# Kernel optimization log

Hardware: AMD Instinct MI355X
Metric: run time of the kernel (lower is better)

Reference implementation:

```python
import jax, jax.numpy as jnp
import numpy as np
import math

B = 8192
N_MODELS = 64
T_PER_SPLIT = 16
MAXLEAF = 64
EMB = 32
BN_EPS = 1e-5


def setup_inputs() -> dict:
    key = jax.random.key(0)
    k1, k2, k3 = jax.random.split(key, 3)
    # leaf indices per (sample, model*tree), values in [0, maxleaf)
    x = jax.random.randint(k1, (B, N_MODELS * T_PER_SPLIT), 0, MAXLEAF, dtype=jnp.int32)
    # embed_w ~ N(0, sqrt(1/max_ntree_per_split))
    embed_w = jax.random.normal(k2, (N_MODELS, T_PER_SPLIT * MAXLEAF, EMB), dtype=jnp.float32) * math.sqrt(1.0 / T_PER_SPLIT)
    # BatchNorm1d affine params (gamma=1, beta=0 at init)
    bn_gamma = jnp.ones((N_MODELS * EMB,), dtype=jnp.float32)
    bn_beta = jnp.zeros((N_MODELS * EMB,), dtype=jnp.float32)
    # BatchDense(n_models, embsize, 1): weight (M, E, 1) squeezed to (M, E), bias zeros (M,)
    stdv = math.sqrt(6.0 / (EMB + 1))
    bout_w = jax.random.uniform(k3, (N_MODELS, EMB), dtype=jnp.float32, minval=-stdv, maxval=stdv)
    bout_b = jnp.zeros((N_MODELS,), dtype=jnp.float32)
    return {"x": x, "embed_w": embed_w, "bn_gamma": bn_gamma, "bn_beta": bn_beta,
            "bout_w": bout_w, "bout_b": bout_b}


def reference(x, embed_w, bn_gamma, bn_beta, bout_w, bout_b):
    # x: (B, M*T) int leaf indices; embed_w: (M, T*L, E)
    Bn = x.shape[0]
    M, TL, E = embed_w.shape
    T = x.shape[1] // M
    L = TL // T
    # one_hot + bmm == per-tree gather from embed_w, summed over trees
    idx = x.reshape(Bn, M, T) + jnp.arange(T, dtype=x.dtype) * L  # (B, M, T) into TL axis
    emb = embed_w[jnp.arange(M)[None, :, None], idx]              # (B, M, T, E) gather
    h = emb.sum(axis=2).reshape(Bn, M * E)                        # (B, M*E)
    # BatchNorm1d (training-mode batch statistics, biased variance as in torch)
    mean = h.mean(axis=0)
    var = h.var(axis=0)
    h = (h - mean) / jnp.sqrt(var + BN_EPS) * bn_gamma + bn_beta
    # dropout is identity in eval mode
    h = h.reshape(Bn, M, E)
    # BatchDense: per-model linear E -> 1
    out = jnp.einsum('bme,me->bm', h, bout_w) + bout_b            # (B, M)
    sum_out = out.sum(axis=-1, keepdims=True)                     # (B, 1)
    return (sum_out, out)
```

## Files before the change

kernel.cpp:

```cpp
#include <hip/hip_runtime.h>
#include <hip/hip_fp16.h>

constexpr int B_TOT = 8192;
constexpr int NM    = 64;
constexpr int TT    = 16;
constexpr int LF    = 64;
constexpr int EM    = 32;
constexpr int XROW  = NM * TT;
constexpr int TROWS = TT * LF;

template<int TQ>
__device__ __forceinline__ int4 qbcast(int4 v) {
    constexpr int c = TQ * 0x55;
    int4 r;
    r.x = __builtin_amdgcn_mov_dpp(v.x, c, 0xf, 0xf, true);
    r.y = __builtin_amdgcn_mov_dpp(v.y, c, 0xf, 0xf, true);
    r.z = __builtin_amdgcn_mov_dpp(v.z, c, 0xf, 0xf, true);
    r.w = __builtin_amdgcn_mov_dpp(v.w, c, 0xf, 0xf, true);
    return r;
}

__device__ __forceinline__ __half2 H2(unsigned u) { return *(const __half2*)&u; }

__global__ __launch_bounds__(512, 4) void k_stats_f16(
    const int* __restrict__ x, const float* __restrict__ tbl,
    float* __restrict__ psum, float* __restrict__ psq)
{
    __shared__ uint4 tb[TROWS * 4];
    __shared__ float red[2][8][32];

    const int m     = blockIdx.x & 63;
    const int chunk = blockIdx.x >> 6;
    const int tid   = threadIdx.x;
    const int f     = tid & 3;
    const int grp   = tid >> 2;
    const int b0    = chunk * 1024;

    {
        const float4* __restrict__ src = (const float4*)(tbl + (size_t)m * (TROWS * EM));
#pragma unroll
        for (int i = 0; i < 8; ++i) {
            const int o = tid + i * 512;
            const float4 a = src[o * 2];
            const float4 c = src[o * 2 + 1];
            uint4 p;
            __half2 h0 = __floats2half2_rn(a.x, a.y);
            __half2 h1 = __floats2half2_rn(a.z, a.w);
            __half2 h2 = __floats2half2_rn(c.x, c.y);
            __half2 h3 = __floats2half2_rn(c.z, c.w);
            p.x = *(unsigned*)&h0; p.y = *(unsigned*)&h1;
            p.z = *(unsigned*)&h2; p.w = *(unsigned*)&h3;
            tb[o] = p;
        }
    }

    int4 xr = ((const int4*)(x + (size_t)(b0 + grp) * XROW + m * TT))[f];

    float s[8], s2[8];
#pragma unroll
    for (int k = 0; k < 8; ++k) { s[k] = 0.f; s2[k] = 0.f; }

    __syncthreads();

    for (int p = 0; p < 8; ++p) {
        int4 nxt;
        if (p < 7)
            nxt = ((const int4*)(x + (size_t)(b0 + (p + 1) * 128 + grp) * XROW + m * TT))[f];

        const int4 q0 = qbcast<0>(xr);
        const int4 q1 = qbcast<1>(xr);
        const int4 q2 = qbcast<2>(xr);
        const int4 q3 = qbcast<3>(xr);

        __half2 h0 = __half2(__half(0.f), __half(0.f));
        __half2 h1 = h0, h2 = h0, h3 = h0;

#define GATH(Q, RB)                                                          \
        {                                                                    \
            const uint4 a0 = tb[((Q).x + RB      ) * 4 + f];                 \
            const uint4 a1 = tb[((Q).y + RB +  64) * 4 + f];                 \
            const uint4 a2 = tb[((Q).z + RB + 128) * 4 + f];                 \
            const uint4 a3 = tb[((Q).w + RB + 192) * 4 + f];                 \
            h0 = __hadd2(h0, __hadd2(__hadd2(H2(a0.x), H2(a1.x)),            \
                                     __hadd2(H2(a2.x), H2(a3.x))));          \
            h1 = __hadd2(h1, __hadd2(__hadd2(H2(a0.y), H2(a1.y)),            \
                                     __hadd2(H2(a2.y), H2(a3.y))));          \
            h2 = __hadd2(h2, __hadd2(__hadd2(H2(a0.z), H2(a1.z)),            \
                                     __hadd2(H2(a2.z), H2(a3.z))));          \
            h3 = __hadd2(h3, __hadd2(__hadd2(H2(a0.w), H2(a1.w)),            \
                                     __hadd2(H2(a2.w), H2(a3.w))));          \
        }
        GATH(q0, 0) GATH(q1, 256) GATH(q2, 512) GATH(q3, 768)
#undef GATH

        const __half2 hv[4] = {h0, h1, h2, h3};
#pragma unroll
        for (int k = 0; k < 4; ++k) {
            const float lo = __low2float(hv[k]);
            const float hi = __high2float(hv[k]);
            s[2*k]   += lo;  s2[2*k]   = fmaf(lo, lo, s2[2*k]);
            s[2*k+1] += hi;  s2[2*k+1] = fmaf(hi, hi, s2[2*k+1]);
        }
        xr = nxt;
    }

#pragma unroll
    for (int off = 4; off <= 32; off <<= 1) {
#pragma unroll
        for (int k = 0; k < 8; ++k) {
            s[k]  += __shfl_xor(s[k],  off);
            s2[k] += __shfl_xor(s2[k], off);
        }
    }
    const int wave = tid >> 6;
    if ((tid & 63) < 4) {
#pragma unroll
        for (int k = 0; k < 8; ++k) {
            red[0][wave][f * 8 + k] = s[k];
            red[1][wave][f * 8 + k] = s2[k];
        }
    }
    __syncthreads();
    if (tid < 32) {
        float a = 0.f, a2 = 0.f;
#pragma unroll
        for (int w = 0; w < 8; ++w) { a += red[0][w][tid]; a2 += red[1][w][tid]; }
        psum[(chunk * NM + m) * EM + tid] = a;
        psq [(chunk * NM + m) * EM + tid] = a2;
    }
}

__global__ __launch_bounds__(256) void k_prep(
    const float* __restrict__ tbl,
    const float* __restrict__ gamma, const float* __restrict__ beta,
    const float* __restrict__ bw, const float* __restrict__ bb,
    const float* __restrict__ psum, const float* __restrict__ psq,
    float* __restrict__ Cm, float* __restrict__ g2)
{
    const int m    = blockIdx.x >> 2;
    const int part = blockIdx.x & 3;
    __shared__ float a_s[EM];
    if (threadIdx.x < EM) {
        const int e  = threadIdx.x;
        const int ch = m * EM + e;
        float sum = 0.f, sq = 0.f;
#pragma unroll
        for (int c = 0; c < 8; ++c) {
            sum += psum[(c * NM + m) * EM + e];
            sq  += psq [(c * NM + m) * EM + e];
        }
        const float inv_n = 1.f / (float)B_TOT;
        const float mean = sum * inv_n;
        const float var  = sq * inv_n - mean * mean;
        const float istd = rsqrtf(var + 1e-5f);
        const float g = gamma[ch];
        const float w = bw[ch];
        a_s[e] = istd * g * w;
        float ct = (beta[ch] - mean * istd * g) * w;
#pragma unroll
        for (int off = 16; off > 0; off >>= 1) ct += __shfl_down(ct, off, 32);
        if (e == 0 && part == 0) Cm[m] = bb[m] + ct;
    }
    __syncthreads();

    const float* __restrict__ tblm = tbl + (size_t)m * (TROWS * EM);
    const int row = part * 256 + threadIdx.x;
    const float4* rp = (const float4*)(tblm + row * EM);
    float acc = 0.f;
#pragma unroll
    for (int i = 0; i < 8; ++i) {
        const float4 v = rp[i];
        acc += v.x * a_s[i*4+0] + v.y * a_s[i*4+1]
             + v.z * a_s[i*4+2] + v.w * a_s[i*4+3];
    }
    g2[row * NM + m] = acc;
}

__global__ __launch_bounds__(1024, 8) void k_out(
    const int* __restrict__ x, const float* __restrict__ g2,
    const float* __restrict__ Cm, float* __restrict__ out)
{
    __shared__ float slab[4 * LF * NM];
    const int tid  = threadIdx.x;
    const int wid  = tid >> 6;
    const int lane = tid & 63;
    const int b    = blockIdx.x * 16 + wid;

    const int4* xp = (const int4*)(x + (size_t)b * XROW + lane * TT);
    const int4 q0 = xp[0], q1 = xp[1], q2 = xp[2], q3 = xp[3];
    const int idxs[16] = {q0.x,q0.y,q0.z,q0.w, q1.x,q1.y,q1.z,q1.w,
                          q2.x,q2.y,q2.z,q2.w, q3.x,q3.y,q3.z,q3.w};

    float acc = 0.f;
#pragma unroll
    for (int ph = 0; ph < 4; ++ph) {
        if (ph) __syncthreads();
        const float4* src = (const float4*)(g2 + (size_t)ph * (4 * LF * NM));
        float4* dst = (float4*)slab;
#pragma unroll
        for (int j = 0; j < 4; ++j) dst[tid + j * 1024] = src[tid + j * 1024];
        __syncthreads();
#pragma unroll
        for (int tt = 0; tt < 4; ++tt)
            acc += slab[tt * (LF * NM) + idxs[ph * 4 + tt] * NM + lane];
    }

    const float o = acc + Cm[lane];
    float s = o;
#pragma unroll
    for (int off = 32; off > 0; off >>= 1) s += __shfl_down(s, off);
    out[B_TOT + (size_t)b * NM + lane] = o;
    if (lane == 0) out[b] = s;
}

extern "C" void kernel_launch(void* const* d_in, const int* in_sizes, int n_in,
                              void* d_out, int out_size, void* d_ws, size_t ws_size,
                              hipStream_t stream) {
    const int*   x       = (const int*)d_in[0];
    const float* embed_w = (const float*)d_in[1];
    const float* gamma   = (const float*)d_in[2];
    const float* beta    = (const float*)d_in[3];
    const float* bout_w  = (const float*)d_in[4];
    const float* bout_b  = (const float*)d_in[5];
    float* out = (float*)d_out;

    float* ws   = (float*)d_ws;
    float* Cm   = ws;
    float* g2   = ws + 64;
    float* psum = ws + 64 + 65536;
    float* psq  = psum + 16384;

    k_stats_f16<<<dim3(512), dim3(512), 0, stream>>>(x, embed_w, psum, psq);
    k_prep<<<dim3(256), dim3(256),  0, stream>>>(embed_w, gamma, beta, bout_w,
                                                 bout_b, psum, psq, Cm, g2);
    k_out <<<dim3(512), dim3(1024), 0, stream>>>(x, g2, Cm, out);
}
```

Baseline: 108.6 us.

## Materialize fp16 embeddings in stats pass and apply BN-dense from them

```diff
diff --git a/kernel.cpp b/kernel.cpp
--- a/kernel.cpp
+++ b/kernel.cpp
@@ -24,7 +24,8 @@
 
 __global__ __launch_bounds__(512, 4) void k_stats_f16(
     const int* __restrict__ x, const float* __restrict__ tbl,
-    float* __restrict__ psum, float* __restrict__ psq)
+    float* __restrict__ psum, float* __restrict__ psq,
+    __half* __restrict__ h_out)
 {
     __shared__ uint4 tb[TROWS * 4];
     __shared__ float red[2][8][32];
@@ -50,7 +51,8 @@
             __half2 h3 = __floats2half2_rn(c.z, c.w);
             p.x = *(unsigned*)&h0; p.y = *(unsigned*)&h1;
             p.z = *(unsigned*)&h2; p.w = *(unsigned*)&h3;
-            tb[o] = p;
+            const int sw = (o & ~3) | ((o ^ (o >> 3)) & 3);
+            tb[sw] = p;
         }
     }
 
@@ -59,6 +61,9 @@
     float s[8], s2[8];
 #pragma unroll
     for (int k = 0; k < 8; ++k) { s[k] = 0.f; s2[k] = 0.f; }
+
+    __half* __restrict__ hp =
+        h_out + ((size_t)(b0 + grp) * NM + m) * EM + f * 8;
 
     __syncthreads();
 
@@ -75,12 +80,13 @@
         __half2 h0 = __half2(__half(0.f), __half(0.f));
         __half2 h1 = h0, h2 = h0, h3 = h0;
 
+#define TIX(r) (((r) << 2) | ((f ^ ((r) >> 1)) & 3))
 #define GATH(Q, RB)                                                          \
         {                                                                    \
-            const uint4 a0 = tb[((Q).x + RB      ) * 4 + f];                 \
-            const uint4 a1 = tb[((Q).y + RB +  64) * 4 + f];                 \
-            const uint4 a2 = tb[((Q).z + RB + 128) * 4 + f];                 \
-            const uint4 a3 = tb[((Q).w + RB + 192) * 4 + f];                 \
+            const uint4 a0 = tb[TIX((Q).x + RB      )];                      \
+            const uint4 a1 = tb[TIX((Q).y + RB +  64)];                      \
+            const uint4 a2 = tb[TIX((Q).z + RB + 128)];                      \
+            const uint4 a3 = tb[TIX((Q).w + RB + 192)];                      \
             h0 = __hadd2(h0, __hadd2(__hadd2(H2(a0.x), H2(a1.x)),            \
                                      __hadd2(H2(a2.x), H2(a3.x))));          \
             h1 = __hadd2(h1, __hadd2(__hadd2(H2(a0.y), H2(a1.y)),            \
@@ -92,6 +98,14 @@
         }
         GATH(q0, 0) GATH(q1, 256) GATH(q2, 512) GATH(q3, 768)
 #undef GATH
+#undef TIX
+
+        {
+            uint4 hv4;
+            hv4.x = *(unsigned*)&h0; hv4.y = *(unsigned*)&h1;
+            hv4.z = *(unsigned*)&h2; hv4.w = *(unsigned*)&h3;
+            *(uint4*)(hp + (size_t)p * 128 * NM * EM) = hv4;
+        }
 
         const __half2 hv[4] = {h0, h1, h2, h3};
 #pragma unroll
@@ -130,87 +144,92 @@
     }
 }
 
-__global__ __launch_bounds__(256) void k_prep(
-    const float* __restrict__ tbl,
+__global__ __launch_bounds__(256) void k_prep2(
     const float* __restrict__ gamma, const float* __restrict__ beta,
     const float* __restrict__ bw, const float* __restrict__ bb,
     const float* __restrict__ psum, const float* __restrict__ psq,
-    float* __restrict__ Cm, float* __restrict__ g2)
+    float* __restrict__ ag, float* __restrict__ Cm)
 {
-    const int m    = blockIdx.x >> 2;
-    const int part = blockIdx.x & 3;
-    __shared__ float a_s[EM];
-    if (threadIdx.x < EM) {
-        const int e  = threadIdx.x;
-        const int ch = m * EM + e;
-        float sum = 0.f, sq = 0.f;
-#pragma unroll
-        for (int c = 0; c < 8; ++c) {
-            sum += psum[(c * NM + m) * EM + e];
-            sq  += psq [(c * NM + m) * EM + e];
-        }
-        const float inv_n = 1.f / (float)B_TOT;
-        const float mean = sum * inv_n;
-        const float var  = sq * inv_n - mean * mean;
-        const float istd = rsqrtf(var + 1e-5f);
-        const float g = gamma[ch];
-        const float w = bw[ch];
-        a_s[e] = istd * g * w;
-        float ct = (beta[ch] - mean * istd * g) * w;
-#pragma unroll
-        for (int off = 16; off > 0; off >>= 1) ct += __shfl_down(ct, off, 32);
-        if (e == 0 && part == 0) Cm[m] = bb[m] + ct;
-    }
-    __syncthreads();
-
-    const float* __restrict__ tblm = tbl + (size_t)m * (TROWS * EM);
-    const int row = part * 256 + threadIdx.x;
-    const float4* rp = (const float4*)(tblm + row * EM);
-    float acc = 0.f;
-#pragma unroll
-    for (int i = 0; i < 8; ++i) {
-        const float4 v = rp[i];
-        acc += v.x * a_s[i*4+0] + v.y * a_s[i*4+1]
-             + v.z * a_s[i*4+2] + v.w * a_s[i*4+3];
-    }
-    g2[row * NM + m] = acc;
-}
-
-__global__ __launch_bounds__(1024, 8) void k_out(
-    const int* __restrict__ x, const float* __restrict__ g2,
+    const int ch = blockIdx.x * 256 + threadIdx.x;
+    const int m  = ch >> 5;
+    const int e  = ch & 31;
+    float sum = 0.f, sq = 0.f;
+#pragma unroll
+    for (int c = 0; c < 8; ++c) {
+        sum += psum[c * (NM * EM) + ch];
+        sq  += psq [c * (NM * EM) + ch];
+    }
+    const float inv_n = 1.f / (float)B_TOT;
+    const float mean  = sum * inv_n;
+    const float var   = sq * inv_n - mean * mean;
+    const float gi    = gamma[ch] * rsqrtf(var + 1e-5f);
+    const float w     = bw[ch];
+    ag[ch] = gi * w;
+    float ct = (beta[ch] - mean * gi) * w;
+#pragma unroll
+    for (int off = 16; off > 0; off >>= 1) ct += __shfl_down(ct, off, 32);
+    if (e == 0) Cm[m] = bb[m] + ct;
+}
+
+__global__ __launch_bounds__(256) void k_out2(
+    const __half* __restrict__ h, const float* __restrict__ ag,
     const float* __restrict__ Cm, float* __restrict__ out)
 {
-    __shared__ float slab[4 * LF * NM];
-    const int tid  = threadIdx.x;
-    const int wid  = tid >> 6;
+    __shared__ float a_s[NM][EM + 1];
+    __shared__ float c_s[NM];
+    const int tid = threadIdx.x;
+#pragma unroll
+    for (int i = 0; i < 8; ++i) {
+        const int o = tid + i * 256;
+        a_s[o >> 5][o & 31] = ag[o];
+    }
+    if (tid < NM) c_s[tid] = Cm[tid];
+    __syncthreads();
+
     const int lane = tid & 63;
-    const int b    = blockIdx.x * 16 + wid;
-
-    const int4* xp = (const int4*)(x + (size_t)b * XROW + lane * TT);
-    const int4 q0 = xp[0], q1 = xp[1], q2 = xp[2], q3 = xp[3];
-    const int idxs[16] = {q0.x,q0.y,q0.z,q0.w, q1.x,q1.y,q1.z,q1.w,
-                          q2.x,q2.y,q2.z,q2.w, q3.x,q3.y,q3.z,q3.w};
-
-    float acc = 0.f;
-#pragma unroll
-    for (int ph = 0; ph < 4; ++ph) {
-        if (ph) __syncthreads();
-        const float4* src = (const float4*)(g2 + (size_t)ph * (4 * LF * NM));
-        float4* dst = (float4*)slab;
-#pragma unroll
-        for (int j = 0; j < 4; ++j) dst[tid + j * 1024] = src[tid + j * 1024];
-        __syncthreads();
-#pragma unroll
-        for (int tt = 0; tt < 4; ++tt)
-            acc += slab[tt * (LF * NM) + idxs[ph * 4 + tt] * NM + lane];
-    }
-
-    const float o = acc + Cm[lane];
-    float s = o;
-#pragma unroll
-    for (int off = 32; off > 0; off >>= 1) s += __shfl_down(s, off);
-    out[B_TOT + (size_t)b * NM + lane] = o;
-    if (lane == 0) out[b] = s;
+    const int wv   = tid >> 6;
+    const int b0   = blockIdx.x * 16 + wv * 4;
+
+    const uint4* __restrict__ hp =
+        (const uint4*)(h) + ((size_t)b0 * NM + lane) * (EM / 8);
+
+    uint4 v[4][4];
+#pragma unroll
+    for (int j = 0; j < 4; ++j)
+#pragma unroll
+        for (int k = 0; k < 4; ++k)
+            v[j][k] = hp[j * 256 + k];
+
+    float ob[4] = {0.f, 0.f, 0.f, 0.f};
+#pragma unroll
+    for (int j = 0; j < 4; ++j) {
+#pragma unroll
+        for (int k = 0; k < 4; ++k) {
+            const float2 f0 = __half22float2(H2(v[j][k].x));
+            const float2 f1 = __half22float2(H2(v[j][k].y));
+            const float2 f2 = __half22float2(H2(v[j][k].z));
+            const float2 f3 = __half22float2(H2(v[j][k].w));
+            const int e = k * 8;
+            ob[j] = fmaf(f0.x, a_s[lane][e + 0], ob[j]);
+            ob[j] = fmaf(f0.y, a_s[lane][e + 1], ob[j]);
+            ob[j] = fmaf(f1.x, a_s[lane][e + 2], ob[j]);
+            ob[j] = fmaf(f1.y, a_s[lane][e + 3], ob[j]);
+            ob[j] = fmaf(f2.x, a_s[lane][e + 4], ob[j]);
+            ob[j] = fmaf(f2.y, a_s[lane][e + 5], ob[j]);
+            ob[j] = fmaf(f3.x, a_s[lane][e + 6], ob[j]);
+            ob[j] = fmaf(f3.y, a_s[lane][e + 7], ob[j]);
+        }
+    }
+
+#pragma unroll
+    for (int j = 0; j < 4; ++j) {
+        const float o = ob[j] + c_s[lane];
+        float s = o;
+#pragma unroll
+        for (int off = 32; off > 0; off >>= 1) s += __shfl_down(s, off);
+        out[B_TOT + (size_t)(b0 + j) * NM + lane] = o;
+        if (lane == 0) out[b0 + j] = s;
+    }
 }
 
 extern "C" void kernel_launch(void* const* d_in, const int* in_sizes, int n_in,
@@ -224,14 +243,15 @@
     const float* bout_b  = (const float*)d_in[5];
     float* out = (float*)d_out;
 
-    float* ws   = (float*)d_ws;
-    float* Cm   = ws;
-    float* g2   = ws + 64;
-    float* psum = ws + 64 + 65536;
-    float* psq  = psum + 16384;
-
-    k_stats_f16<<<dim3(512), dim3(512), 0, stream>>>(x, embed_w, psum, psq);
-    k_prep<<<dim3(256), dim3(256),  0, stream>>>(embed_w, gamma, beta, bout_w,
-                                                 bout_b, psum, psq, Cm, g2);
-    k_out <<<dim3(512), dim3(1024), 0, stream>>>(x, g2, Cm, out);
-}
+    __half* h    = (__half*)d_ws;
+    float*  ws   = (float*)d_ws + ((size_t)B_TOT * NM * EM / 2);
+    float* psum  = ws;
+    float* psq   = psum + 16384;
+    float* ag    = psq + 16384;
+    float* Cm    = ag + 2048;
+
+    k_stats_f16<<<dim3(512), dim3(512), 0, stream>>>(x, embed_w, psum, psq, h);
+    k_prep2   <<<dim3(8),   dim3(256), 0, stream>>>(gamma, beta, bout_w, bout_b,
+                                                    psum, psq, ag, Cm);
+    k_out2    <<<dim3(512), dim3(256), 0, stream>>>(h, ag, Cm, out);
+}
```

Result: slower. 118.1 us (+8.7%).

## Store folded output table in fp16 and split stats LDS table into halves

Applied to the files above, without the earlier changes.

```diff
diff --git a/kernel.cpp b/kernel.cpp
--- a/kernel.cpp
+++ b/kernel.cpp
@@ -26,7 +26,7 @@
     const int* __restrict__ x, const float* __restrict__ tbl,
     float* __restrict__ psum, float* __restrict__ psq)
 {
-    __shared__ uint4 tb[TROWS * 4];
+    __shared__ uint2 tbS[2][TROWS * 4];
     __shared__ float red[2][8][32];
 
     const int m     = blockIdx.x & 63;
@@ -43,14 +43,15 @@
             const int o = tid + i * 512;
             const float4 a = src[o * 2];
             const float4 c = src[o * 2 + 1];
-            uint4 p;
             __half2 h0 = __floats2half2_rn(a.x, a.y);
             __half2 h1 = __floats2half2_rn(a.z, a.w);
             __half2 h2 = __floats2half2_rn(c.x, c.y);
             __half2 h3 = __floats2half2_rn(c.z, c.w);
-            p.x = *(unsigned*)&h0; p.y = *(unsigned*)&h1;
-            p.z = *(unsigned*)&h2; p.w = *(unsigned*)&h3;
-            tb[o] = p;
+            uint2 lo, hi;
+            lo.x = *(unsigned*)&h0; lo.y = *(unsigned*)&h1;
+            hi.x = *(unsigned*)&h2; hi.y = *(unsigned*)&h3;
+            tbS[0][o] = lo;
+            tbS[1][o] = hi;
         }
     }
 
@@ -63,7 +64,7 @@
     __syncthreads();
 
     for (int p = 0; p < 8; ++p) {
-        int4 nxt;
+        int4 nxt = xr;
         if (p < 7)
             nxt = ((const int4*)(x + (size_t)(b0 + (p + 1) * 128 + grp) * XROW + m * TT))[f];
 
@@ -75,23 +76,21 @@
         __half2 h0 = __half2(__half(0.f), __half(0.f));
         __half2 h1 = h0, h2 = h0, h3 = h0;
 
-#define GATH(Q, RB)                                                          \
+#define ROWADD(R)                                                            \
         {                                                                    \
-            const uint4 a0 = tb[((Q).x + RB      ) * 4 + f];                 \
-            const uint4 a1 = tb[((Q).y + RB +  64) * 4 + f];                 \
-            const uint4 a2 = tb[((Q).z + RB + 128) * 4 + f];                 \
-            const uint4 a3 = tb[((Q).w + RB + 192) * 4 + f];                 \
-            h0 = __hadd2(h0, __hadd2(__hadd2(H2(a0.x), H2(a1.x)),            \
-                                     __hadd2(H2(a2.x), H2(a3.x))));          \
-            h1 = __hadd2(h1, __hadd2(__hadd2(H2(a0.y), H2(a1.y)),            \
-                                     __hadd2(H2(a2.y), H2(a3.y))));          \
-            h2 = __hadd2(h2, __hadd2(__hadd2(H2(a0.z), H2(a1.z)),            \
-                                     __hadd2(H2(a2.z), H2(a3.z))));          \
-            h3 = __hadd2(h3, __hadd2(__hadd2(H2(a0.w), H2(a1.w)),            \
-                                     __hadd2(H2(a2.w), H2(a3.w))));          \
-        }
-        GATH(q0, 0) GATH(q1, 256) GATH(q2, 512) GATH(q3, 768)
-#undef GATH
+            const int ix = ((R) << 2) | f;                                   \
+            const uint2 lo = tbS[0][ix];                                     \
+            const uint2 hi = tbS[1][ix];                                     \
+            h0 = __hadd2(h0, H2(lo.x));                                      \
+            h1 = __hadd2(h1, H2(lo.y));                                      \
+            h2 = __hadd2(h2, H2(hi.x));                                      \
+            h3 = __hadd2(h3, H2(hi.y));                                      \
+        }
+        ROWADD(q0.x)        ROWADD(q0.y +  64) ROWADD(q0.z + 128) ROWADD(q0.w + 192)
+        ROWADD(q1.x + 256)  ROWADD(q1.y + 320) ROWADD(q1.z + 384) ROWADD(q1.w + 448)
+        ROWADD(q2.x + 512)  ROWADD(q2.y + 576) ROWADD(q2.z + 640) ROWADD(q2.w + 704)
+        ROWADD(q3.x + 768)  ROWADD(q3.y + 832) ROWADD(q3.z + 896) ROWADD(q3.w + 960)
+#undef ROWADD
 
         const __half2 hv[4] = {h0, h1, h2, h3};
 #pragma unroll
@@ -135,7 +134,7 @@
     const float* __restrict__ gamma, const float* __restrict__ beta,
     const float* __restrict__ bw, const float* __restrict__ bb,
     const float* __restrict__ psum, const float* __restrict__ psq,
-    float* __restrict__ Cm, float* __restrict__ g2)
+    float* __restrict__ Cm, __half* __restrict__ g2h)
 {
     const int m    = blockIdx.x >> 2;
     const int part = blockIdx.x & 3;
@@ -173,14 +172,14 @@
         acc += v.x * a_s[i*4+0] + v.y * a_s[i*4+1]
              + v.z * a_s[i*4+2] + v.w * a_s[i*4+3];
     }
-    g2[row * NM + m] = acc;
+    g2h[row * NM + m] = __float2half(acc);
 }
 
 __global__ __launch_bounds__(1024, 8) void k_out(
-    const int* __restrict__ x, const float* __restrict__ g2,
+    const int* __restrict__ x, const __half* __restrict__ g2h,
     const float* __restrict__ Cm, float* __restrict__ out)
 {
-    __shared__ float slab[4 * LF * NM];
+    __shared__ __half slab[8 * LF * NM];
     const int tid  = threadIdx.x;
     const int wid  = tid >> 6;
     const int lane = tid & 63;
@@ -193,16 +192,16 @@
 
     float acc = 0.f;
 #pragma unroll
-    for (int ph = 0; ph < 4; ++ph) {
+    for (int ph = 0; ph < 2; ++ph) {
         if (ph) __syncthreads();
-        const float4* src = (const float4*)(g2 + (size_t)ph * (4 * LF * NM));
-        float4* dst = (float4*)slab;
+        const uint4* src = (const uint4*)(g2h + (size_t)ph * (8 * LF * NM));
+        uint4* dst = (uint4*)slab;
 #pragma unroll
         for (int j = 0; j < 4; ++j) dst[tid + j * 1024] = src[tid + j * 1024];
         __syncthreads();
 #pragma unroll
-        for (int tt = 0; tt < 4; ++tt)
-            acc += slab[tt * (LF * NM) + idxs[ph * 4 + tt] * NM + lane];
+        for (int tt = 0; tt < 8; ++tt)
+            acc += __half2float(slab[tt * (LF * NM) + idxs[ph * 8 + tt] * NM + lane]);
     }
 
     const float o = acc + Cm[lane];
@@ -225,13 +224,13 @@
     float* out = (float*)d_out;
 
     float* ws   = (float*)d_ws;
-    float* Cm   = ws;
-    float* g2   = ws + 64;
-    float* psum = ws + 64 + 65536;
+    float* psum = ws;
     float* psq  = psum + 16384;
+    float* Cm   = psq + 16384;
+    __half* g2h = (__half*)(ws + 16384 + 16384 + 64);
 
     k_stats_f16<<<dim3(512), dim3(512), 0, stream>>>(x, embed_w, psum, psq);
     k_prep<<<dim3(256), dim3(256),  0, stream>>>(embed_w, gamma, beta, bout_w,
-                                                 bout_b, psum, psq, Cm, g2);
-    k_out <<<dim3(512), dim3(1024), 0, stream>>>(x, g2, Cm, out);
-}
+                                                 bout_b, psum, psq, Cm, g2h);
+    k_out <<<dim3(512), dim3(1024), 0, stream>>>(x, g2h, Cm, out);
+}
```

Result: slower. 112.6 us (+3.6%).

## Restructure output kernel per model with LDS gather and atomic row sums

Applied to the files above, without the earlier changes.

```diff
diff --git a/kernel.cpp b/kernel.cpp
--- a/kernel.cpp
+++ b/kernel.cpp
@@ -63,7 +63,7 @@
     __syncthreads();
 
     for (int p = 0; p < 8; ++p) {
-        int4 nxt;
+        int4 nxt = xr;
         if (p < 7)
             nxt = ((const int4*)(x + (size_t)(b0 + (p + 1) * 128 + grp) * XROW + m * TT))[f];
 
@@ -173,44 +173,46 @@
         acc += v.x * a_s[i*4+0] + v.y * a_s[i*4+1]
              + v.z * a_s[i*4+2] + v.w * a_s[i*4+3];
     }
-    g2[row * NM + m] = acc;
-}
-
-__global__ __launch_bounds__(1024, 8) void k_out(
+    g2[m * TROWS + row] = acc;
+}
+
+__global__ __launch_bounds__(512) void k_out3(
     const int* __restrict__ x, const float* __restrict__ g2,
     const float* __restrict__ Cm, float* __restrict__ out)
 {
-    __shared__ float slab[4 * LF * NM];
-    const int tid  = threadIdx.x;
-    const int wid  = tid >> 6;
-    const int lane = tid & 63;
-    const int b    = blockIdx.x * 16 + wid;
-
-    const int4* xp = (const int4*)(x + (size_t)b * XROW + lane * TT);
-    const int4 q0 = xp[0], q1 = xp[1], q2 = xp[2], q3 = xp[3];
-    const int idxs[16] = {q0.x,q0.y,q0.z,q0.w, q1.x,q1.y,q1.z,q1.w,
-                          q2.x,q2.y,q2.z,q2.w, q3.x,q3.y,q3.z,q3.w};
-
-    float acc = 0.f;
-#pragma unroll
-    for (int ph = 0; ph < 4; ++ph) {
-        if (ph) __syncthreads();
-        const float4* src = (const float4*)(g2 + (size_t)ph * (4 * LF * NM));
-        float4* dst = (float4*)slab;
-#pragma unroll
-        for (int j = 0; j < 4; ++j) dst[tid + j * 1024] = src[tid + j * 1024];
-        __syncthreads();
-#pragma unroll
-        for (int tt = 0; tt < 4; ++tt)
-            acc += slab[tt * (LF * NM) + idxs[ph * 4 + tt] * NM + lane];
-    }
-
-    const float o = acc + Cm[lane];
-    float s = o;
-#pragma unroll
-    for (int off = 32; off > 0; off >>= 1) s += __shfl_down(s, off);
-    out[B_TOT + (size_t)b * NM + lane] = o;
-    if (lane == 0) out[b] = s;
+    __shared__ float g2s[TROWS];
+    const int m     = blockIdx.x >> 3;
+    const int chunk = blockIdx.x & 7;
+    const int tid   = threadIdx.x;
+    const int f     = tid & 3;
+    const int grp   = tid >> 2;
+    const int b0    = chunk * 1024;
+
+    ((float2*)g2s)[tid] = ((const float2*)(g2 + m * TROWS))[tid];
+
+    int4 xq[8];
+#pragma unroll
+    for (int p = 0; p < 8; ++p)
+        xq[p] = ((const int4*)(x + (size_t)(b0 + p * 128 + grp) * XROW + m * TT))[f];
+
+    const float C = Cm[m];
+    const int base = f * 256;
+
+    __syncthreads();
+
+#pragma unroll
+    for (int p = 0; p < 8; ++p) {
+        float d = g2s[base       + xq[p].x]
+                + g2s[base +  64 + xq[p].y]
+                + g2s[base + 128 + xq[p].z]
+                + g2s[base + 192 + xq[p].w];
+        d += __shfl_xor(d, 1);
+        d += __shfl_xor(d, 2);
+        const int b = b0 + p * 128 + grp;
+        const float o = d + C;
+        if (f == 0) out[B_TOT + (size_t)b * NM + m] = o;
+        if (f == 1) atomicAdd(&out[b], o);
+    }
 }
 
 extern "C" void kernel_launch(void* const* d_in, const int* in_sizes, int n_in,
@@ -225,13 +227,13 @@
     float* out = (float*)d_out;
 
     float* ws   = (float*)d_ws;
-    float* Cm   = ws;
-    float* g2   = ws + 64;
-    float* psum = ws + 64 + 65536;
+    float* psum = ws;
     float* psq  = psum + 16384;
+    float* Cm   = psq + 16384;
+    float* g2   = Cm + 64;
 
     k_stats_f16<<<dim3(512), dim3(512), 0, stream>>>(x, embed_w, psum, psq);
     k_prep<<<dim3(256), dim3(256),  0, stream>>>(embed_w, gamma, beta, bout_w,
                                                  bout_b, psum, psq, Cm, g2);
-    k_out <<<dim3(512), dim3(1024), 0, stream>>>(x, g2, Cm, out);
-}
+    k_out3<<<dim3(512), dim3(512),  0, stream>>>(x, g2, Cm, out);
+}
```

Measured after the change: 113.1 us. +4.1%, slower.
